# Optimization experiments

Hardware: AMD Instinct MI355X
Metric: run time of the kernel (lower is better)

## Reference

```python
import math
import jax, jax.numpy as jnp
import numpy as np

DIM = 2048
N_HEADS = 16
HEAD_DIM = DIM // N_HEADS  # 128
BSZ = 2
SEQLEN = 2048
ROPE_THETA = 500000.0


def _make_freqs(seqlen, head_dim, theta):
    inv = 1.0 / (theta ** (np.arange(0, head_dim, 2, dtype=np.float32) / head_dim))
    t = np.arange(seqlen, dtype=np.float32)
    f = np.outer(t, inv)  # [S, hd//2]
    return jnp.asarray(np.cos(f)), jnp.asarray(np.sin(f))


def setup_inputs() -> dict:
    key = jax.random.key(0)
    kx, kq, kk, kv, ko = jax.random.split(key, 5)
    scale = 0.02
    x = jax.random.normal(kx, (BSZ, SEQLEN, DIM), dtype=jnp.float32)
    wq = jax.random.normal(kq, (DIM, DIM), dtype=jnp.float32) * scale
    wk = jax.random.normal(kk, (DIM, DIM), dtype=jnp.float32) * scale
    wv = jax.random.normal(kv, (DIM, DIM), dtype=jnp.float32) * scale
    wo = jax.random.normal(ko, (DIM, DIM), dtype=jnp.float32) * scale
    freqs_cos, freqs_sin = _make_freqs(SEQLEN, HEAD_DIM, ROPE_THETA)
    # causal additive mask: 0 on/below diag, -inf above
    mask = jnp.triu(jnp.full((SEQLEN, SEQLEN), float('-inf'), dtype=jnp.float32), k=1)
    return {"x": x, "start_pos": 0, "freqs_cos": freqs_cos, "freqs_sin": freqs_sin,
            "mask": mask, "wq": wq, "wk": wk, "wv": wv, "wo": wo}


def _apply_rope(t, cos, sin):
    # t: [B, S, H, hd]; cos/sin: [S, hd//2]
    b, s, h, hd = t.shape
    tr = t.reshape(b, s, h, hd // 2, 2)
    a, bb = tr[..., 0], tr[..., 1]
    c = cos[None, :, None, :]
    sn = sin[None, :, None, :]
    out_r = a * c - bb * sn
    out_i = a * sn + bb * c
    return jnp.stack([out_r, out_i], axis=-1).reshape(b, s, h, hd)


def reference(x, start_pos, freqs_cos, freqs_sin, mask, wq, wk, wv, wo):
    b, s, _ = x.shape
    xq = (x @ wq.T).reshape(b, s, N_HEADS, HEAD_DIM)
    xk = (x @ wk.T).reshape(b, s, N_HEADS, HEAD_DIM)
    xv = (x @ wv.T).reshape(b, s, N_HEADS, HEAD_DIM)
    xq = _apply_rope(xq, freqs_cos, freqs_sin)
    xk = _apply_rope(xk, freqs_cos, freqs_sin)
    # [B, H, S, hd]
    xq = xq.transpose(0, 2, 1, 3)
    xk = xk.transpose(0, 2, 1, 3)
    xv = xv.transpose(0, 2, 1, 3)
    scores = jnp.einsum('bhqd,bhkd->bhqk', xq, xk) / math.sqrt(HEAD_DIM)
    scores = scores + mask[None, None, :, :]
    probs = jax.nn.softmax(scores.astype(jnp.float32), axis=-1).astype(xq.dtype)
    out = jnp.einsum('bhqk,bhkd->bhqd', probs, xv)
    out = out.transpose(0, 2, 1, 3).reshape(b, s, -1)
    return out @ wo.T
```

## Files before the change

### kernel.cpp

```cpp
#include <hip/hip_runtime.h>
#include <stdint.h>

#define DIM 2048
#define SEQ 2048
#define NHEADS 16
#define HDIM 128
#define BSZ 2
#define ROWS (BSZ*SEQ)

typedef uint16_t u16;
typedef __attribute__((ext_vector_type(8))) short bf16x8;
typedef __attribute__((ext_vector_type(4))) short bf16x4;
typedef __attribute__((ext_vector_type(4))) float fx4;
typedef __attribute__((ext_vector_type(4))) uint16_t u16x4;

typedef const __attribute__((address_space(1))) uint32_t* gp_t;
typedef __attribute__((address_space(3))) uint32_t* lp_t;
#define GLL16(g, l) __builtin_amdgcn_global_load_lds((gp_t)(g), (lp_t)(l), 16, 0, 0)

__device__ inline u16 f2bf(float f) {
  union { float f; uint32_t u; } v; v.f = f;
  uint32_t u = v.u;
  u += 0x7FFFu + ((u >> 16) & 1u);
  return (u16)(u >> 16);
}
__device__ inline float bf2f(u16 h) {
  union { uint32_t u; float f; } v; v.u = ((uint32_t)h) << 16;
  return v.f;
}

__global__ __launch_bounds__(256) void cvt5_kernel(const float* __restrict__ sx,
    const float* __restrict__ s1, const float* __restrict__ s2,
    const float* __restrict__ s3, const float* __restrict__ s4,
    u16* __restrict__ dst) {
  const int XC = (ROWS * DIM) / 4;
  const int WC = (DIM * DIM) / 4;
  int i = blockIdx.x * 256 + threadIdx.x;
  const float* src;
  int off;
  if (i < XC) { src = sx; off = i; }
  else {
    int t = i - XC;
    int w = t >> 20;
    off = t & (WC - 1);
    src = (w == 0) ? s1 : (w == 1) ? s2 : (w == 2) ? s3 : s4;
  }
  fx4 f = *(const fx4*)(src + (size_t)off * 4);
  u16x4 o;
  o[0] = f2bf(f[0]); o[1] = f2bf(f[1]); o[2] = f2bf(f[2]); o[3] = f2bf(f[3]);
  *(u16x4*)(dst + (size_t)i * 4) = o;
}

#define BM 256
#define BN 128
#define BK 64
#define NT (DIM / BK)
#define BUFSZ ((BM + BN) * BK)

__global__ __launch_bounds__(512, 2) void gemm_qkv8(const u16* __restrict__ A,
    const u16* __restrict__ B0, const u16* __restrict__ B1, const u16* __restrict__ B2,
    u16* __restrict__ C0, u16* __restrict__ C1, u16* __restrict__ vtg,
    const float* __restrict__ fcos, const float* __restrict__ fsin) {
  __shared__ __align__(16) u16 sm[2 * BUFSZ];

  const int tid  = threadIdx.x;
  const int lane = tid & 63, wave = tid >> 6;
  const int l16  = lane & 15, quad = lane >> 4;
  const int wm   = wave >> 2;
  const int wn   = wave & 3;

  int t = (blockIdx.x & 7) * 96 + (blockIdx.x >> 3);
  const int z   = t >> 8;
  const int rem = t & 255;
  const int M0  = (rem >> 4) * BM;
  const int N0  = (rem & 15) * BN;
  const u16* B = (z == 0) ? B0 : (z == 1) ? B1 : B2;

  const int u0 = tid, u1 = 512 + tid;
  const int rl0 = u0 >> 3, ch0 = (u0 & 7) ^ (rl0 & 7);
  const int rl1 = u1 >> 3, ch1 = (u1 & 7) ^ (rl1 & 7);

  const int sw  = l16 & 7;
  const int ka0 = (quad ^ sw) * 8;
  const int ka1 = ((4 + quad) ^ sw) * 8;
  const int rowA = (wm * 128 + l16) * BK;
  const int rowB = (wn * 32  + l16) * BK;

#define STGA(h, kt2) do { if ((kt2) < NT) {                                              \
    const u16* _g = A + (size_t)(M0 + (h) * 128) * DIM + (kt2) * BK;                     \
    u16* _l = sm + ((kt2) & 1) * BUFSZ + (h) * 8192 + wave * 512;                        \
    GLL16(_g + (size_t)rl0 * DIM + ch0 * 8, _l);                                         \
    GLL16(_g + (size_t)rl1 * DIM + ch1 * 8, _l + 4096); } } while (0)
#define STGB(kt2) do { if ((kt2) < NT) {                                                 \
    const u16* _g = B + (size_t)N0 * DIM + (kt2) * BK;                                   \
    u16* _l = sm + ((kt2) & 1) * BUFSZ + 16384 + wave * 512;                             \
    GLL16(_g + (size_t)rl0 * DIM + ch0 * 8, _l);                                         \
    GLL16(_g + (size_t)rl1 * DIM + ch1 * 8, _l + 4096); } } while (0)

  STGB(0); STGA(0, 0); STGA(1, 0);
  STGB(1); STGA(0, 1);
  asm volatile("s_waitcnt vmcnt(4)" ::: "memory");
  __builtin_amdgcn_s_barrier();

  fx4 acc[8][2];
#pragma unroll
  for (int m = 0; m < 8; ++m)
#pragma unroll
    for (int n = 0; n < 2; ++n) acc[m][n] = fx4{0.f, 0.f, 0.f, 0.f};

  bf16x8 af[4][2], b0[2], b1[2];

  for (int kt = 0; kt < NT; ++kt) {
    const u16* Ab = sm + (kt & 1) * BUFSZ;
    const u16* Bb = Ab + 16384;

#pragma unroll
    for (int m = 0; m < 4; ++m) {
      af[m][0] = *(const bf16x8*)(Ab + rowA + m * (16 * BK) + ka0);
      af[m][1] = *(const bf16x8*)(Ab + rowA + m * (16 * BK) + ka1);
    }
    b0[0] = *(const bf16x8*)(Bb + rowB + ka0);
    b0[1] = *(const bf16x8*)(Bb + rowB + ka1);
    STGA(1, kt + 1);
    asm volatile("s_waitcnt lgkmcnt(8)" ::: "memory");
    __builtin_amdgcn_sched_barrier(0);
    __builtin_amdgcn_s_barrier();
    asm volatile("s_waitcnt lgkmcnt(0)" ::: "memory");
    __builtin_amdgcn_sched_barrier(0);
    __builtin_amdgcn_s_setprio(1);
#pragma unroll
    for (int m = 0; m < 4; ++m) {
      acc[m][0] = __builtin_amdgcn_mfma_f32_16x16x32_bf16(af[m][0], b0[0], acc[m][0], 0, 0, 0);
      acc[m][0] = __builtin_amdgcn_mfma_f32_16x16x32_bf16(af[m][1], b0[1], acc[m][0], 0, 0, 0);
    }
    __builtin_amdgcn_s_setprio(0);
    __builtin_amdgcn_s_barrier();

    b1[0] = *(const bf16x8*)(Bb + rowB + 16 * BK + ka0);
    b1[1] = *(const bf16x8*)(Bb + rowB + 16 * BK + ka1);
    __builtin_amdgcn_s_barrier();
    asm volatile("s_waitcnt lgkmcnt(0)" ::: "memory");
    __builtin_amdgcn_sched_barrier(0);
    __builtin_amdgcn_s_setprio(1);
#pragma unroll
    for (int m = 0; m < 4; ++m) {
      acc[m][1] = __builtin_amdgcn_mfma_f32_16x16x32_bf16(af[m][0], b1[0], acc[m][1], 0, 0, 0);
      acc[m][1] = __builtin_amdgcn_mfma_f32_16x16x32_bf16(af[m][1], b1[1], acc[m][1], 0, 0, 0);
    }
    __builtin_amdgcn_s_setprio(0);
    __builtin_amdgcn_s_barrier();

#pragma unroll
    for (int m = 0; m < 4; ++m) {
      af[m][0] = *(const bf16x8*)(Ab + rowA + (m + 4) * (16 * BK) + ka0);
      af[m][1] = *(const bf16x8*)(Ab + rowA + (m + 4) * (16 * BK) + ka1);
    }
    STGB(kt + 2);
    __builtin_amdgcn_s_barrier();
    asm volatile("s_waitcnt lgkmcnt(0)" ::: "memory");
    __builtin_amdgcn_sched_barrier(0);
    __builtin_amdgcn_s_setprio(1);
#pragma unroll
    for (int m = 0; m < 4; ++m) {
      acc[m + 4][1] = __builtin_amdgcn_mfma_f32_16x16x32_bf16(af[m][0], b1[0], acc[m + 4][1], 0, 0, 0);
      acc[m + 4][1] = __builtin_amdgcn_mfma_f32_16x16x32_bf16(af[m][1], b1[1], acc[m + 4][1], 0, 0, 0);
    }
    __builtin_amdgcn_s_setprio(0);
    __builtin_amdgcn_s_barrier();

    STGA(0, kt + 2);
    __builtin_amdgcn_s_barrier();
    __builtin_amdgcn_s_setprio(1);
#pragma unroll
    for (int m = 0; m < 4; ++m) {
      acc[m + 4][0] = __builtin_amdgcn_mfma_f32_16x16x32_bf16(af[m][0], b0[0], acc[m + 4][0], 0, 0, 0);
      acc[m + 4][0] = __builtin_amdgcn_mfma_f32_16x16x32_bf16(af[m][1], b0[1], acc[m + 4][0], 0, 0, 0);
    }
    __builtin_amdgcn_s_setprio(0);
    if (kt < NT - 2) asm volatile("s_waitcnt vmcnt(4)" ::: "memory");
    else             asm volatile("s_waitcnt vmcnt(0)" ::: "memory");
    __builtin_amdgcn_sched_barrier(0);
    __builtin_amdgcn_s_barrier();
  }
#undef STGA
#undef STGB

  if (z < 2) {
    u16* C = (z == 0) ? C0 : C1;
    u16* Cr = C + (size_t)(M0 + wm * 128 + quad * 4) * DIM + N0 + wn * 32 + l16;
#pragma unroll
    for (int mt = 0; mt < 8; ++mt)
#pragma unroll
      for (int r = 0; r < 4; ++r) {
        int s = (M0 + wm * 128 + mt * 16 + quad * 4 + r) & (SEQ - 1);
        const float* cb = fcos + s * 64;
        const float* sb = fsin + s * 64;
#pragma unroll
        for (int nt = 0; nt < 2; ++nt) {
          int p = (wn * 32 + nt * 16 + l16) >> 1;
          float val = acc[mt][nt][r];
          float par = __shfl_xor(val, 1);
          float c = cb[p], sn = sb[p];
          float out = (l16 & 1) ? (par * sn + val * c) : (val * c - par * sn);
          Cr[(size_t)(mt * 16 + r) * DIM + nt * 16] = f2bf(out);
        }
      }
  } else {
    u16 (*T)[256] = reinterpret_cast<u16 (*)[256]>(sm);
    __syncthreads();
#pragma unroll
    for (int mt = 0; mt < 8; ++mt)
#pragma unroll
      for (int nt = 0; nt < 2; ++nt) {
        int col = wn * 32 + nt * 16 + l16;
        int rowb = (wm * 128 + mt * 16 + quad * 4) ^ ((col & 7) << 3);
        u16x4 p;
        p[0] = f2bf(acc[mt][nt][0]); p[1] = f2bf(acc[mt][nt][1]);
        p[2] = f2bf(acc[mt][nt][2]); p[3] = f2bf(acc[mt][nt][3]);
        *(u16x4*)&T[col][rowb] = p;
      }
    __syncthreads();
    const int b  = M0 >> 11;
    const int s0 = M0 & (SEQ - 1);
    const int h  = N0 >> 7;
#pragma unroll
    for (int i = 0; i < 8; ++i) {
      int c = i * 512 + tid;
      int col = c >> 5;
      int s8 = (c & 31) * 8;
      bf16x8 v8 = *(const bf16x8*)&T[col][s8 ^ ((col & 7) << 3)];
      *(bf16x8*)(vtg + ((size_t)(b * NHEADS + h) * HDIM + col) * SEQ + s0 + s8) = v8;
    }
  }
}

__global__ __launch_bounds__(512, 2) void gemm_out8(const u16* __restrict__ A,
                                                    const u16* __restrict__ B,
                                                    float* __restrict__ C) {
  __shared__ __align__(16) u16 sm[2 * BUFSZ];

  const int tid  = threadIdx.x;
  const int lane = tid & 63, wave = tid >> 6;
  const int l16  = lane & 15, quad = lane >> 4;
  const int wm   = wave >> 2;
  const int wn   = wave & 3;

  int t = (blockIdx.x & 7) * 32 + (blockIdx.x >> 3);
  const int M0  = (t >> 4) * BM;
  const int N0  = (t & 15) * BN;

  const int u0 = tid, u1 = 512 + tid;
  const int rl0 = u0 >> 3, ch0 = (u0 & 7) ^ (rl0 & 7);
  const int rl1 = u1 >> 3, ch1 = (u1 & 7) ^ (rl1 & 7);

  const int sw  = l16 & 7;
  const int ka0 = (quad ^ sw) * 8;
  const int ka1 = ((4 + quad) ^ sw) * 8;
  const int rowA = (wm * 128 + l16) * BK;
  const int rowB = (wn * 32  + l16) * BK;

#define STGA(h, kt2) do { if ((kt2) < NT) {                                              \
    const u16* _g = A + (size_t)(M0 + (h) * 128) * DIM + (kt2) * BK;                     \
    u16* _l = sm + ((kt2) & 1) * BUFSZ + (h) * 8192 + wave * 512;                        \
    GLL16(_g + (size_t)rl0 * DIM + ch0 * 8, _l);                                         \
    GLL16(_g + (size_t)rl1 * DIM + ch1 * 8, _l + 4096); } } while (0)
#define STGB(kt2) do { if ((kt2) < NT) {                                                 \
    const u16* _g = B + (size_t)N0 * DIM + (kt2) * BK;                                   \
    u16* _l = sm + ((kt2) & 1) * BUFSZ + 16384 + wave * 512;                             \
    GLL16(_g + (size_t)rl0 * DIM + ch0 * 8, _l);                                         \
    GLL16(_g + (size_t)rl1 * DIM + ch1 * 8, _l + 4096); } } while (0)

  STGB(0); STGA(0, 0); STGA(1, 0);
  STGB(1); STGA(0, 1);
  asm volatile("s_waitcnt vmcnt(4)" ::: "memory");
  __builtin_amdgcn_s_barrier();

  fx4 acc[8][2];
#pragma unroll
  for (int m = 0; m < 8; ++m)
#pragma unroll
    for (int n = 0; n < 2; ++n) acc[m][n] = fx4{0.f, 0.f, 0.f, 0.f};

  bf16x8 af[4][2], b0[2], b1[2];

  for (int kt = 0; kt < NT; ++kt) {
    const u16* Ab = sm + (kt & 1) * BUFSZ;
    const u16* Bb = Ab + 16384;

#pragma unroll
    for (int m = 0; m < 4; ++m) {
      af[m][0] = *(const bf16x8*)(Ab + rowA + m * (16 * BK) + ka0);
      af[m][1] = *(const bf16x8*)(Ab + rowA + m * (16 * BK) + ka1);
    }
    b0[0] = *(const bf16x8*)(Bb + rowB + ka0);
    b0[1] = *(const bf16x8*)(Bb + rowB + ka1);
    STGA(1, kt + 1);
    asm volatile("s_waitcnt lgkmcnt(8)" ::: "memory");
    __builtin_amdgcn_sched_barrier(0);
    __builtin_amdgcn_s_barrier();
    asm volatile("s_waitcnt lgkmcnt(0)" ::: "memory");
    __builtin_amdgcn_sched_barrier(0);
    __builtin_amdgcn_s_setprio(1);
#pragma unroll
    for (int m = 0; m < 4; ++m) {
      acc[m][0] = __builtin_amdgcn_mfma_f32_16x16x32_bf16(af[m][0], b0[0], acc[m][0], 0, 0, 0);
      acc[m][0] = __builtin_amdgcn_mfma_f32_16x16x32_bf16(af[m][1], b0[1], acc[m][0], 0, 0, 0);
    }
    __builtin_amdgcn_s_setprio(0);
    __builtin_amdgcn_s_barrier();

    b1[0] = *(const bf16x8*)(Bb + rowB + 16 * BK + ka0);
    b1[1] = *(const bf16x8*)(Bb + rowB + 16 * BK + ka1);
    __builtin_amdgcn_s_barrier();
    asm volatile("s_waitcnt lgkmcnt(0)" ::: "memory");
    __builtin_amdgcn_sched_barrier(0);
    __builtin_amdgcn_s_setprio(1);
#pragma unroll
    for (int m = 0; m < 4; ++m) {
      acc[m][1] = __builtin_amdgcn_mfma_f32_16x16x32_bf16(af[m][0], b1[0], acc[m][1], 0, 0, 0);
      acc[m][1] = __builtin_amdgcn_mfma_f32_16x16x32_bf16(af[m][1], b1[1], acc[m][1], 0, 0, 0);
    }
    __builtin_amdgcn_s_setprio(0);
    __builtin_amdgcn_s_barrier();

#pragma unroll
    for (int m = 0; m < 4; ++m) {
      af[m][0] = *(const bf16x8*)(Ab + rowA + (m + 4) * (16 * BK) + ka0);
      af[m][1] = *(const bf16x8*)(Ab + rowA + (m + 4) * (16 * BK) + ka1);
    }
    STGB(kt + 2);
    __builtin_amdgcn_s_barrier();
    asm volatile("s_waitcnt lgkmcnt(0)" ::: "memory");
    __builtin_amdgcn_sched_barrier(0);
    __builtin_amdgcn_s_setprio(1);
#pragma unroll
    for (int m = 0; m < 4; ++m) {
      acc[m + 4][1] = __builtin_amdgcn_mfma_f32_16x16x32_bf16(af[m][0], b1[0], acc[m + 4][1], 0, 0, 0);
      acc[m + 4][1] = __builtin_amdgcn_mfma_f32_16x16x32_bf16(af[m][1], b1[1], acc[m + 4][1], 0, 0, 0);
    }
    __builtin_amdgcn_s_setprio(0);
    __builtin_amdgcn_s_barrier();

    STGA(0, kt + 2);
    __builtin_amdgcn_s_barrier();
    __builtin_amdgcn_s_setprio(1);
#pragma unroll
    for (int m = 0; m < 4; ++m) {
      acc[m + 4][0] = __builtin_amdgcn_mfma_f32_16x16x32_bf16(af[m][0], b0[0], acc[m + 4][0], 0, 0, 0);
      acc[m + 4][0] = __builtin_amdgcn_mfma_f32_16x16x32_bf16(af[m][1], b0[1], acc[m + 4][0], 0, 0, 0);
    }
    __builtin_amdgcn_s_setprio(0);
    if (kt < NT - 2) asm volatile("s_waitcnt vmcnt(4)" ::: "memory");
    else             asm volatile("s_waitcnt vmcnt(0)" ::: "memory");
    __builtin_amdgcn_sched_barrier(0);
    __builtin_amdgcn_s_barrier();
  }
#undef STGA
#undef STGB

  float* Cr = C + (size_t)(M0 + wm * 128 + quad * 4) * DIM + N0 + wn * 32 + l16;
#pragma unroll
  for (int mt = 0; mt < 8; ++mt)
#pragma unroll
    for (int nt = 0; nt < 2; ++nt)
#pragma unroll
      for (int r = 0; r < 4; ++r)
        Cr[(size_t)(mt * 16 + r) * DIM + nt * 16] = acc[mt][nt][r];
}

struct SMemS { u16 Ks[2][64][136]; u16 Vt[2][128][72]; };
union SMemU { SMemS s; u16 Ot[4][32][136]; };

__global__ __launch_bounds__(256, 2) void attn_kernel(const u16* __restrict__ qm,
                                                      const u16* __restrict__ km,
                                                      const u16* __restrict__ vtg,
                                                      u16* __restrict__ ao) {
  __shared__ __align__(16) SMemU sm;
  const int tid = threadIdx.x;
  const int lane = tid & 63, wave = tid >> 6;
  const int l16 = lane & 15, quad = lane >> 4;
  const int idx = blockIdx.x;
  const int bh = idx & 31;
  const int j = idx >> 5;
  const int qt = (j < 8) ? (15 - j) : (j - 8);
  const int b = bh >> 4, h = bh & 15;
  const int q0 = qt * 128;
  const size_t brow = (size_t)b * SEQ;
  const int hc = h * HDIM;
  const size_t vbase = (size_t)bh * HDIM * SEQ;
  const int nkt = 2 * qt + 2;

  bf16x8 aq[2][4];
#pragma unroll
  for (int nt = 0; nt < 2; ++nt) {
    size_t qbase = (brow + q0 + wave * 32 + nt * 16 + l16) * DIM + hc;
#pragma unroll
    for (int dc = 0; dc < 4; ++dc)
      aq[nt][dc] = *(const bf16x8*)(qm + qbase + dc * 32 + quad * 8);
  }
  fx4 o[2][8];
#pragma unroll
  for (int nt = 0; nt < 2; ++nt)
#pragma unroll
    for (int dt = 0; dt < 8; ++dt) o[nt][dt] = fx4{0.f, 0.f, 0.f, 0.f};
  float mr[2] = {-3e38f, -3e38f}, lr[2] = {0.f, 0.f};

  bf16x8 kreg[4], vreg[4];
#pragma unroll
  for (int i = 0; i < 4; ++i) {
    int c = i * 256 + tid;
    kreg[i] = *(const bf16x8*)(km + (brow + (c >> 4)) * DIM + hc + (c & 15) * 8);
    vreg[i] = *(const bf16x8*)(vtg + vbase + (size_t)(c >> 3) * SEQ + (c & 7) * 8);
  }
#pragma unroll
  for (int i = 0; i < 4; ++i) {
    int c = i * 256 + tid;
    *(bf16x8*)&sm.s.Ks[0][c >> 4][(c & 15) * 8] = kreg[i];
    *(bf16x8*)&sm.s.Vt[0][c >> 3][(c & 7) * 8] = vreg[i];
  }
  if (1 < nkt) {
#pragma unroll
    for (int i = 0; i < 4; ++i) {
      int c = i * 256 + tid;
      kreg[i] = *(const bf16x8*)(km + (brow + 64 + (c >> 4)) * DIM + hc + (c & 15) * 8);
      vreg[i] = *(const bf16x8*)(vtg + vbase + (size_t)(c >> 3) * SEQ + 64 + (c & 7) * 8);
    }
  }
  __syncthreads();

  for (int kt = 0; kt < nkt; ++kt) {
    const int cur = kt & 1;
    if (kt + 1 < nkt) {
#pragma unroll
      for (int i = 0; i < 4; ++i) {
        int c = i * 256 + tid;
        *(bf16x8*)&sm.s.Ks[cur ^ 1][c >> 4][(c & 15) * 8] = kreg[i];
        *(bf16x8*)&sm.s.Vt[cur ^ 1][c >> 3][(c & 7) * 8] = vreg[i];
      }
    }
    if (kt + 2 < nkt) {
      const int kv2 = (kt + 2) * 64;
#pragma unroll
      for (int i = 0; i < 4; ++i) {
        int c = i * 256 + tid;
        kreg[i] = *(const bf16x8*)(km + (brow + kv2 + (c >> 4)) * DIM + hc + (c & 15) * 8);
        vreg[i] = *(const bf16x8*)(vtg + vbase + (size_t)(c >> 3) * SEQ + kv2 + (c & 7) * 8);
      }
    }
    fx4 s[2][4];
#pragma unroll
    for (int tm = 0; tm < 4; ++tm) {
      fx4 a0 = fx4{0.f, 0.f, 0.f, 0.f}, a1 = fx4{0.f, 0.f, 0.f, 0.f};
#pragma unroll
      for (int dc = 0; dc < 4; ++dc) {
        bf16x8 kf = *(const bf16x8*)&sm.s.Ks[cur][tm * 16 + l16][dc * 32 + quad * 8];
        a0 = __builtin_amdgcn_mfma_f32_16x16x32_bf16(kf, aq[0][dc], a0, 0, 0, 0);
        a1 = __builtin_amdgcn_mfma_f32_16x16x32_bf16(kf, aq[1][dc], a1, 0, 0, 0);
      }
      s[0][tm] = a0 * 0.08838834764831845f;
      s[1][tm] = a1 * 0.08838834764831845f;
    }
    if (kt >= nkt - 2) {
      const int kv0 = kt * 64;
#pragma unroll
      for (int nt = 0; nt < 2; ++nt) {
        int qpos = q0 + wave * 32 + nt * 16 + l16;
#pragma unroll
        for (int tm = 0; tm < 4; ++tm)
#pragma unroll
          for (int r = 0; r < 4; ++r)
            if (kv0 + tm * 16 + quad * 4 + r > qpos) s[nt][tm][r] = -1e30f;
      }
    }
    bf16x4 pf[2][4];
#pragma unroll
    for (int nt = 0; nt < 2; ++nt) {
      float t = -3e38f;
#pragma unroll
      for (int tm = 0; tm < 4; ++tm)
        t = fmaxf(t, fmaxf(fmaxf(s[nt][tm][0], s[nt][tm][1]),
                           fmaxf(s[nt][tm][2], s[nt][tm][3])));
      t = fmaxf(t, __shfl_xor(t, 16));
      t = fmaxf(t, __shfl_xor(t, 32));
      if (!__all(t - mr[nt] <= 8.f)) {
        float mnew = fmaxf(mr[nt], t);
        float alpha = __expf(mr[nt] - mnew);
        lr[nt] *= alpha;
        mr[nt] = mnew;
#pragma unroll
        for (int dt = 0; dt < 8; ++dt) o[nt][dt] *= alpha;
      }
      float sum = 0.f;
#pragma unroll
      for (int tm = 0; tm < 4; ++tm) {
        fx4 p;
#pragma unroll
        for (int r = 0; r < 4; ++r) {
          p[r] = __expf(s[nt][tm][r] - mr[nt]);
          sum += p[r];
        }
        bf16x4 pb;
        pb[0] = (short)f2bf(p[0]); pb[1] = (short)f2bf(p[1]);
        pb[2] = (short)f2bf(p[2]); pb[3] = (short)f2bf(p[3]);
        pf[nt][tm] = pb;
      }
      sum += __shfl_xor(sum, 16);
      sum += __shfl_xor(sum, 32);
      lr[nt] += sum;
    }
#pragma unroll
    for (int tm = 0; tm < 4; ++tm) {
#pragma unroll
      for (int dt = 0; dt < 8; ++dt) {
        bf16x4 vf = *(const bf16x4*)&sm.s.Vt[cur][dt * 16 + l16][tm * 16 + quad * 4];
        o[0][dt] = __builtin_amdgcn_mfma_f32_16x16x16bf16_1k(vf, pf[0][tm], o[0][dt], 0, 0, 0);
        o[1][dt] = __builtin_amdgcn_mfma_f32_16x16x16bf16_1k(vf, pf[1][tm], o[1][dt], 0, 0, 0);
      }
    }
    __syncthreads();
  }
#pragma unroll
  for (int nt = 0; nt < 2; ++nt) {
    float inv = 1.f / lr[nt];
#pragma unroll
    for (int dt = 0; dt < 8; ++dt) {
      fx4 v = o[nt][dt];
      u16x4 p;
      p[0] = f2bf(v[0] * inv); p[1] = f2bf(v[1] * inv);
      p[2] = f2bf(v[2] * inv); p[3] = f2bf(v[3] * inv);
      *(u16x4*)&sm.Ot[wave][nt * 16 + l16][dt * 16 + quad * 4] = p;
    }
  }
#pragma unroll
  for (int i = 0; i < 8; ++i) {
    int c = i * 64 + lane;
    int row = c >> 4;
    int ch = c & 15;
    bf16x8 t = *(const bf16x8*)&sm.Ot[wave][row][ch * 8];
    *(bf16x8*)(ao + (brow + q0 + wave * 32 + row) * DIM + hc + ch * 8) = t;
  }
}

extern "C" void kernel_launch(void* const* d_in, const int* in_sizes, int n_in,
                              void* d_out, int out_size, void* d_ws, size_t ws_size,
                              hipStream_t stream) {
  const float* x    = (const float*)d_in[0];
  const float* fcos = (const float*)d_in[2];
  const float* fsin = (const float*)d_in[3];
  const float* wq   = (const float*)d_in[5];
  const float* wk   = (const float*)d_in[6];
  const float* wv   = (const float*)d_in[7];
  const float* wo   = (const float*)d_in[8];
  float* out = (float*)d_out;

  const size_t XN = (size_t)ROWS * DIM;
  const size_t WN = (size_t)DIM * DIM;
  u16* ws  = (u16*)d_ws;
  u16* xb  = ws;
  u16* wqb = xb + XN;
  u16* wkb = wqb + WN;
  u16* wvb = wkb + WN;
  u16* wob = wvb + WN;
  u16* q   = wob + WN;
  u16* k   = q + XN;
  u16* vtg = k + XN;
  u16* ao  = vtg + XN;

  const int total_chunks = (int)((XN + 4 * WN) / 4);
  cvt5_kernel<<<total_chunks / 256, 256, 0, stream>>>(x, wq, wk, wv, wo, ws);

  gemm_qkv8<<<dim3(768), 512, 0, stream>>>(xb, wqb, wkb, wvb, q, k, vtg, fcos, fsin);

  attn_kernel<<<dim3(512), 256, 0, stream>>>(q, k, vtg, ao);

  gemm_out8<<<dim3(256), 512, 0, stream>>>(ao, wob, out);
}
```

Measured before the change: 387.5 us.

## Collapse GEMM inner loop into two phases with upfront LDS fragment loads

Loads all eight A fragments and both B fragments from LDS at the start of each k-step, then runs the MFMAs in two larger phases instead of four interleaved load/compute phases. The prefetch of the next tiles into shared memory is issued together between the two phases, removing several barriers and lgkmcnt waits. This reduces synchronization overhead and gives the matrix units longer uninterrupted runs. In exchange it doubles the fragment registers held live, which may reduce occupancy or cause spills.

```diff
diff --git a/kernel.cpp b/kernel.cpp
--- a/kernel.cpp
+++ b/kernel.cpp
@@ -108,19 +108,21 @@
 #pragma unroll
     for (int n = 0; n < 2; ++n) acc[m][n] = fx4{0.f, 0.f, 0.f, 0.f};
 
-  bf16x8 af[4][2], b0[2], b1[2];
+  bf16x8 af[8][2], b0[2], b1[2];
 
   for (int kt = 0; kt < NT; ++kt) {
     const u16* Ab = sm + (kt & 1) * BUFSZ;
     const u16* Bb = Ab + 16384;
 
 #pragma unroll
-    for (int m = 0; m < 4; ++m) {
+    for (int m = 0; m < 8; ++m) {
       af[m][0] = *(const bf16x8*)(Ab + rowA + m * (16 * BK) + ka0);
       af[m][1] = *(const bf16x8*)(Ab + rowA + m * (16 * BK) + ka1);
     }
     b0[0] = *(const bf16x8*)(Bb + rowB + ka0);
     b0[1] = *(const bf16x8*)(Bb + rowB + ka1);
+    b1[0] = *(const bf16x8*)(Bb + rowB + 16 * BK + ka0);
+    b1[1] = *(const bf16x8*)(Bb + rowB + 16 * BK + ka1);
     STGA(1, kt + 1);
     asm volatile("s_waitcnt lgkmcnt(8)" ::: "memory");
     __builtin_amdgcn_sched_barrier(0);
@@ -132,49 +134,21 @@
     for (int m = 0; m < 4; ++m) {
       acc[m][0] = __builtin_amdgcn_mfma_f32_16x16x32_bf16(af[m][0], b0[0], acc[m][0], 0, 0, 0);
       acc[m][0] = __builtin_amdgcn_mfma_f32_16x16x32_bf16(af[m][1], b0[1], acc[m][0], 0, 0, 0);
+      acc[m][1] = __builtin_amdgcn_mfma_f32_16x16x32_bf16(af[m][0], b1[0], acc[m][1], 0, 0, 0);
+      acc[m][1] = __builtin_amdgcn_mfma_f32_16x16x32_bf16(af[m][1], b1[1], acc[m][1], 0, 0, 0);
     }
     __builtin_amdgcn_s_setprio(0);
     __builtin_amdgcn_s_barrier();
 
-    b1[0] = *(const bf16x8*)(Bb + rowB + 16 * BK + ka0);
-    b1[1] = *(const bf16x8*)(Bb + rowB + 16 * BK + ka1);
-    __builtin_amdgcn_s_barrier();
-    asm volatile("s_waitcnt lgkmcnt(0)" ::: "memory");
-    __builtin_amdgcn_sched_barrier(0);
+    STGB(kt + 2);
+    STGA(0, kt + 2);
     __builtin_amdgcn_s_setprio(1);
 #pragma unroll
     for (int m = 0; m < 4; ++m) {
-      acc[m][1] = __builtin_amdgcn_mfma_f32_16x16x32_bf16(af[m][0], b1[0], acc[m][1], 0, 0, 0);
-      acc[m][1] = __builtin_amdgcn_mfma_f32_16x16x32_bf16(af[m][1], b1[1], acc[m][1], 0, 0, 0);
-    }
-    __builtin_amdgcn_s_setprio(0);
-    __builtin_amdgcn_s_barrier();
-
-#pragma unroll
-    for (int m = 0; m < 4; ++m) {
-      af[m][0] = *(const bf16x8*)(Ab + rowA + (m + 4) * (16 * BK) + ka0);
-      af[m][1] = *(const bf16x8*)(Ab + rowA + (m + 4) * (16 * BK) + ka1);
-    }
-    STGB(kt + 2);
-    __builtin_amdgcn_s_barrier();
-    asm volatile("s_waitcnt lgkmcnt(0)" ::: "memory");
-    __builtin_amdgcn_sched_barrier(0);
-    __builtin_amdgcn_s_setprio(1);
-#pragma unroll
-    for (int m = 0; m < 4; ++m) {
-      acc[m + 4][1] = __builtin_amdgcn_mfma_f32_16x16x32_bf16(af[m][0], b1[0], acc[m + 4][1], 0, 0, 0);
-      acc[m + 4][1] = __builtin_amdgcn_mfma_f32_16x16x32_bf16(af[m][1], b1[1], acc[m + 4][1], 0, 0, 0);
-    }
-    __builtin_amdgcn_s_setprio(0);
-    __builtin_amdgcn_s_barrier();
-
-    STGA(0, kt + 2);
-    __builtin_amdgcn_s_barrier();
-    __builtin_amdgcn_s_setprio(1);
-#pragma unroll
-    for (int m = 0; m < 4; ++m) {
-      acc[m + 4][0] = __builtin_amdgcn_mfma_f32_16x16x32_bf16(af[m][0], b0[0], acc[m + 4][0], 0, 0, 0);
-      acc[m + 4][0] = __builtin_amdgcn_mfma_f32_16x16x32_bf16(af[m][1], b0[1], acc[m + 4][0], 0, 0, 0);
+      acc[m + 4][0] = __builtin_amdgcn_mfma_f32_16x16x32_bf16(af[m + 4][0], b0[0], acc[m + 4][0], 0, 0, 0);
+      acc[m + 4][0] = __builtin_amdgcn_mfma_f32_16x16x32_bf16(af[m + 4][1], b0[1], acc[m + 4][0], 0, 0, 0);
+      acc[m + 4][1] = __builtin_amdgcn_mfma_f32_16x16x32_bf16(af[m + 4][0], b1[0], acc[m + 4][1], 0, 0, 0);
+      acc[m + 4][1] = __builtin_amdgcn_mfma_f32_16x16x32_bf16(af[m + 4][1], b1[1], acc[m + 4][1], 0, 0, 0);
     }
     __builtin_amdgcn_s_setprio(0);
     if (kt < NT - 2) asm volatile("s_waitcnt vmcnt(4)" ::: "memory");
@@ -281,19 +255,21 @@
 #pragma unroll
     for (int n = 0; n < 2; ++n) acc[m][n] = fx4{0.f, 0.f, 0.f, 0.f};
 
-  bf16x8 af[4][2], b0[2], b1[2];
+  bf16x8 af[8][2], b0[2], b1[2];
 
   for (int kt = 0; kt < NT; ++kt) {
     const u16* Ab = sm + (kt & 1) * BUFSZ;
     const u16* Bb = Ab + 16384;
 
 #pragma unroll
-    for (int m = 0; m < 4; ++m) {
+    for (int m = 0; m < 8; ++m) {
       af[m][0] = *(const bf16x8*)(Ab + rowA + m * (16 * BK) + ka0);
       af[m][1] = *(const bf16x8*)(Ab + rowA + m * (16 * BK) + ka1);
     }
     b0[0] = *(const bf16x8*)(Bb + rowB + ka0);
     b0[1] = *(const bf16x8*)(Bb + rowB + ka1);
+    b1[0] = *(const bf16x8*)(Bb + rowB + 16 * BK + ka0);
+    b1[1] = *(const bf16x8*)(Bb + rowB + 16 * BK + ka1);
     STGA(1, kt + 1);
     asm volatile("s_waitcnt lgkmcnt(8)" ::: "memory");
     __builtin_amdgcn_sched_barrier(0);
@@ -305,49 +281,21 @@
     for (int m = 0; m < 4; ++m) {
       acc[m][0] = __builtin_amdgcn_mfma_f32_16x16x32_bf16(af[m][0], b0[0], acc[m][0], 0, 0, 0);
       acc[m][0] = __builtin_amdgcn_mfma_f32_16x16x32_bf16(af[m][1], b0[1], acc[m][0], 0, 0, 0);
+      acc[m][1] = __builtin_amdgcn_mfma_f32_16x16x32_bf16(af[m][0], b1[0], acc[m][1], 0, 0, 0);
+      acc[m][1] = __builtin_amdgcn_mfma_f32_16x16x32_bf16(af[m][1], b1[1], acc[m][1], 0, 0, 0);
     }
     __builtin_amdgcn_s_setprio(0);
     __builtin_amdgcn_s_barrier();
 
-    b1[0] = *(const bf16x8*)(Bb + rowB + 16 * BK + ka0);
-    b1[1] = *(const bf16x8*)(Bb + rowB + 16 * BK + ka1);
-    __builtin_amdgcn_s_barrier();
-    asm volatile("s_waitcnt lgkmcnt(0)" ::: "memory");
-    __builtin_amdgcn_sched_barrier(0);
+    STGB(kt + 2);
+    STGA(0, kt + 2);
     __builtin_amdgcn_s_setprio(1);
 #pragma unroll
     for (int m = 0; m < 4; ++m) {
-      acc[m][1] = __builtin_amdgcn_mfma_f32_16x16x32_bf16(af[m][0], b1[0], acc[m][1], 0, 0, 0);
-      acc[m][1] = __builtin_amdgcn_mfma_f32_16x16x32_bf16(af[m][1], b1[1], acc[m][1], 0, 0, 0);
-    }
-    __builtin_amdgcn_s_setprio(0);
-    __builtin_amdgcn_s_barrier();
-
-#pragma unroll
-    for (int m = 0; m < 4; ++m) {
-      af[m][0] = *(const bf16x8*)(Ab + rowA + (m + 4) * (16 * BK) + ka0);
-      af[m][1] = *(const bf16x8*)(Ab + rowA + (m + 4) * (16 * BK) + ka1);
-    }
-    STGB(kt + 2);
-    __builtin_amdgcn_s_barrier();
-    asm volatile("s_waitcnt lgkmcnt(0)" ::: "memory");
-    __builtin_amdgcn_sched_barrier(0);
-    __builtin_amdgcn_s_setprio(1);
-#pragma unroll
-    for (int m = 0; m < 4; ++m) {
-      acc[m + 4][1] = __builtin_amdgcn_mfma_f32_16x16x32_bf16(af[m][0], b1[0], acc[m + 4][1], 0, 0, 0);
-      acc[m + 4][1] = __builtin_amdgcn_mfma_f32_16x16x32_bf16(af[m][1], b1[1], acc[m + 4][1], 0, 0, 0);
-    }
-    __builtin_amdgcn_s_setprio(0);
-    __builtin_amdgcn_s_barrier();
-
-    STGA(0, kt + 2);
-    __builtin_amdgcn_s_barrier();
-    __builtin_amdgcn_s_setprio(1);
-#pragma unroll
-    for (int m = 0; m < 4; ++m) {
-      acc[m + 4][0] = __builtin_amdgcn_mfma_f32_16x16x32_bf16(af[m][0], b0[0], acc[m + 4][0], 0, 0, 0);
-      acc[m + 4][0] = __builtin_amdgcn_mfma_f32_16x16x32_bf16(af[m][1], b0[1], acc[m + 4][0], 0, 0, 0);
+      acc[m + 4][0] = __builtin_amdgcn_mfma_f32_16x16x32_bf16(af[m + 4][0], b0[0], acc[m + 4][0], 0, 0, 0);
+      acc[m + 4][0] = __builtin_amdgcn_mfma_f32_16x16x32_bf16(af[m + 4][1], b0[1], acc[m + 4][0], 0, 0, 0);
+      acc[m + 4][1] = __builtin_amdgcn_mfma_f32_16x16x32_bf16(af[m + 4][0], b1[0], acc[m + 4][1], 0, 0, 0);
+      acc[m + 4][1] = __builtin_amdgcn_mfma_f32_16x16x32_bf16(af[m + 4][1], b1[1], acc[m + 4][1], 0, 0, 0);
     }
     __builtin_amdgcn_s_setprio(0);
     if (kt < NT - 2) asm volatile("s_waitcnt vmcnt(4)" ::: "memory");
```

Result: no change. 381.6 us (-1.5%).
